# Kernel tuning notes

Measured on AMD Instinct MI355X. Metric: run time of the kernel, lower is better.

Reference implementation:

```python
import jax, jax.numpy as jnp
import numpy as np

IN_C = 256
OUT_C = 256
K = 3
PAD = 1
SCALE = 1.0 / np.sqrt(IN_C * K * K)  # 1/sqrt(in_channels * k^2)
EPS = 1e-8
NEG_SLOPE = 0.2


def setup_inputs() -> dict:
    key = jax.random.key(0)
    k0, k1, k2, k3 = jax.random.split(key, 4)
    B, H, W, SD = 8, 128, 128, 512
    x = jax.random.normal(k0, (B, IN_C, H, W), dtype=jnp.float32)
    style = jax.random.normal(k1, (B, SD), dtype=jnp.float32)
    weight = jax.random.normal(k2, (OUT_C, IN_C, K, K), dtype=jnp.float32)
    mod_w = jax.random.normal(k3, (IN_C, SD), dtype=jnp.float32) / np.sqrt(SD)
    mod_b = jnp.zeros((IN_C,), dtype=jnp.float32)
    return {"x": x, "style": style, "weight": weight, "mod_w": mod_w, "mod_b": mod_b}


def reference(x, style, weight, mod_w, mod_b):
    # modulation: Linear(style_dim -> in_channels)
    s = style @ mod_w.T + mod_b                      # [B, I]
    # per-sample modulated weight [B, O, I, k, k]
    w = SCALE * weight[None] * s[:, None, :, None, None]
    # demodulation over (I, kh, kw)
    demod = jax.lax.rsqrt(jnp.sum(w * w, axis=(2, 3, 4)) + EPS)  # [B, O]
    w = w * demod[:, :, None, None, None]
    # per-sample conv (equivalent to groups=batch trick), vmapped over batch
    def conv_one(xi, wi):  # xi: [I,H,W], wi: [O,I,k,k]
        return jax.lax.conv_general_dilated(
            xi[None], wi, window_strides=(1, 1),
            padding=((PAD, PAD), (PAD, PAD)),
            dimension_numbers=("NCHW", "OIHW", "NCHW"))[0]
    y = jax.vmap(conv_one)(x, w)                     # [B, O, H, W]
    # LeakyReLU(0.2)
    return jnp.where(y >= 0, y, NEG_SLOPE * y)
```

## Files before the change

### kernel.cpp

```cpp
#include <hip/hip_runtime.h>
#include <hip/hip_bf16.h>
#include <cstddef>
#include <cstdint>


#define IN_C 256
#define OUT_C 256
#define HW 16384
#define W_IMG 128
#define SDIM 512
#define SCALE_F 0.020833333333333332f
#define EPS_F 1e-8f
#define NEG_SLOPE 0.2f

#define XROWB 8320
#define WTILEB 8192

typedef short bf16x8 __attribute__((ext_vector_type(8)));
typedef float f32x4 __attribute__((ext_vector_type(4)));

__device__ __forceinline__ unsigned short f2bf(float f) {
  unsigned u = __builtin_bit_cast(unsigned, f);
  unsigned r = u + 0x7FFFu + ((u >> 16) & 1u);
  return (unsigned short)(r >> 16);
}

__device__ __forceinline__ void glds16(const void* g, void* l) {
  __builtin_amdgcn_global_load_lds(
      (const __attribute__((address_space(1))) unsigned int*)g,
      (__attribute__((address_space(3))) unsigned int*)l, 16, 0, 0);
}

__global__ void style_mod_kernel(const float* __restrict__ style,
                                 const float* __restrict__ mod_w,
                                 const float* __restrict__ mod_b,
                                 float* __restrict__ s_out) {
  int b = blockIdx.x;
  int i = threadIdx.x;
  const float* st = style + (size_t)b * SDIM;
  const float* mw = mod_w + (size_t)i * SDIM;
  float acc = 0.f;
#pragma unroll 8
  for (int j = 0; j < SDIM; ++j) acc += st[j] * mw[j];
  s_out[b * IN_C + i] = acc + mod_b[i];
}

__global__ void demod_kernel(const float* __restrict__ weight,
                             const float* __restrict__ s_in,
                             float* __restrict__ dscaled) {
  int bo = blockIdx.x;
  int b = bo >> 8, o = bo & 255;
  int i = threadIdx.x;
  const float* wp = weight + ((size_t)o * IN_C + i) * 9;
  float wsum = 0.f;
#pragma unroll
  for (int k = 0; k < 9; ++k) wsum += wp[k] * wp[k];
  float sv = s_in[b * IN_C + i];
  float v = sv * sv * wsum;
#pragma unroll
  for (int off = 32; off > 0; off >>= 1) v += __shfl_down(v, off);
  __shared__ float red[4];
  int lane = threadIdx.x & 63, wv = threadIdx.x >> 6;
  if (lane == 0) red[wv] = v;
  __syncthreads();
  if (threadIdx.x == 0) {
    float t = red[0] + red[1] + red[2] + red[3];
    dscaled[bo] = SCALE_F * rsqrtf(SCALE_F * SCALE_F * t + EPS_F);
  }
}

__global__ void wpack_kernel(const float* __restrict__ weight,
                             unsigned char* __restrict__ wbf) {
  int tap = blockIdx.x, oblk = blockIdx.y, iblk = blockIdx.z;
  unsigned char* dst = wbf + ((size_t)((tap * 2 + oblk) * 8 + iblk)) * WTILEB;
  for (int t = threadIdx.x; t < 512; t += 256) {
    int oo = t >> 2, c = t & 3;
    int cp = c ^ ((oo >> 1) & 3);
    int o = oblk * 128 + oo;
    bf16x8 v;
#pragma unroll
    for (int j = 0; j < 8; ++j) {
      int i = iblk * 32 + c * 8 + j;
      v[j] = (short)f2bf(weight[((size_t)o * IN_C + i) * 9 + tap]);
    }
    *(bf16x8*)(dst + oo * 64 + cp * 16) = v;
  }
}

__global__ void xpack_kernel(const float* __restrict__ x,
                             const float* __restrict__ s_in,
                             unsigned char* __restrict__ xp) {
  int row = blockIdx.x, iblk = blockIdx.y, b = blockIdx.z;
  const float* xb = x + ((size_t)(b * IN_C + iblk * 32)) * HW + row * W_IMG;
  const float* sb = s_in + b * IN_C + iblk * 32;
  unsigned char* dst = xp + ((size_t)((b * 8 + iblk) * 128 + row)) * XROWB;
  for (int t = threadIdx.x; t < 520; t += 256) {
    int slot = t >> 2, c = t & 3;
    int cp = c ^ ((slot >> 1) & 3);
    int pix = slot - 1;
    bf16x8 v = (bf16x8)(short)0;
    if ((unsigned)pix < 128u) {
#pragma unroll
      for (int j = 0; j < 8; ++j) {
        int ii = c * 8 + j;
        float xv = xb[(size_t)ii * HW + pix];
        v[j] = (short)f2bf(xv * sb[ii]);
      }
    }
    *(bf16x8*)(dst + slot * 64 + cp * 16) = v;
  }
}

__global__ __launch_bounds__(256, 4) void modconv_kernel(
    const unsigned char* __restrict__ xp, const unsigned char* __restrict__ wbf,
    const float* __restrict__ dscaled, float* __restrict__ out) {
  __shared__ __align__(16) unsigned char lds[XROWB + 3 * WTILEB];

  const int tid = threadIdx.x;
  const int lane = tid & 63;
  const int wv = tid >> 6;
  const int wr = wv >> 1, wc = wv & 1;
  const int h = blockIdx.x;
  const int oblk = blockIdx.y;
  const int b = blockIdx.z;
  const int l15 = lane & 15, cc = lane >> 4;

  f32x4 acc[4][4] = {};

  const int axor = ((cc ^ ((l15 >> 1) & 3)) << 4);
  int aoff[4];
#pragma unroll
  for (int m = 0; m < 4; ++m)
    aoff[m] = XROWB + (wr * 64 + m * 16 + l15) * 64 + axor;

  for (int kh = 0; kh < 3; ++kh) {
    const int row = h + kh - 1;
    if ((unsigned)row >= 128u) continue;
    for (int i0 = 0; i0 < 8; ++i0) {
      const unsigned char* xsrc =
          xp + ((size_t)((b * 8 + i0) * 128 + row)) * XROWB;
      for (int tsk = wv; tsk < 33; tsk += 4) {
        if (tsk < 24) {
          int kw = tsk >> 3, ch = tsk & 7;
          const unsigned char* g =
              wbf + ((size_t)(((kh * 3 + kw) * 2 + oblk) * 8 + i0)) * WTILEB +
              ch * 1024 + lane * 16;
          glds16(g, lds + XROWB + kw * WTILEB + ch * 1024);
        } else if (tsk < 32) {
          int ch = tsk - 24;
          glds16(xsrc + ch * 1024 + lane * 16, lds + ch * 1024);
        } else if (lane < 8) {
          glds16(xsrc + 8192 + lane * 16, lds + 8192);
        }
      }
      asm volatile("s_waitcnt vmcnt(0)" ::: "memory");
      __syncthreads();
#pragma unroll
      for (int kw = 0; kw < 3; ++kw) {
        bf16x8 a0 = *(const bf16x8*)(lds + kw * WTILEB + aoff[0]);
        bf16x8 a1 = *(const bf16x8*)(lds + kw * WTILEB + aoff[1]);
        bf16x8 a2 = *(const bf16x8*)(lds + kw * WTILEB + aoff[2]);
        bf16x8 a3 = *(const bf16x8*)(lds + kw * WTILEB + aoff[3]);
        const int bb0 = (wc * 64 + l15 + kw) * 64 +
                        ((cc ^ (((l15 + kw) >> 1) & 3)) << 4);
        __builtin_amdgcn_s_setprio(1);
#pragma unroll
        for (int n = 0; n < 4; ++n) {
          bf16x8 bn = *(const bf16x8*)(lds + bb0 + n * 1024);
          acc[0][n] = __builtin_amdgcn_mfma_f32_16x16x32_bf16(a0, bn, acc[0][n], 0, 0, 0);
          acc[1][n] = __builtin_amdgcn_mfma_f32_16x16x32_bf16(a1, bn, acc[1][n], 0, 0, 0);
          acc[2][n] = __builtin_amdgcn_mfma_f32_16x16x32_bf16(a2, bn, acc[2][n], 0, 0, 0);
          acc[3][n] = __builtin_amdgcn_mfma_f32_16x16x32_bf16(a3, bn, acc[3][n], 0, 0, 0);
        }
        __builtin_amdgcn_s_setprio(0);
      }
      __syncthreads();
    }
  }

  const float* db = dscaled + b * OUT_C + oblk * 128;
  float* ob = out + (((size_t)(b * OUT_C + oblk * 128)) << 14);
  const int pixb = h * 128 + wc * 64 + l15;
#pragma unroll
  for (int m = 0; m < 4; ++m) {
#pragma unroll
    for (int r = 0; r < 4; ++r) {
      int oo = wr * 64 + m * 16 + cc * 4 + r;
      float d = db[oo];
#pragma unroll
      for (int n = 0; n < 4; ++n) {
        float v = acc[m][n][r] * d;
        v = (v >= 0.f) ? v : NEG_SLOPE * v;
        ob[((size_t)oo << 14) + pixb + n * 16] = v;
      }
    }
  }
}

extern "C" void kernel_launch(void* const* d_in, const int* in_sizes, int n_in,
                              void* d_out, int out_size, void* d_ws,
                              size_t ws_size, hipStream_t stream) {
  const float* x = (const float*)d_in[0];
  const float* style = (const float*)d_in[1];
  const float* weight = (const float*)d_in[2];
  const float* mod_w = (const float*)d_in[3];
  const float* mod_b = (const float*)d_in[4];
  float* out = (float*)d_out;

  float* s_ws = (float*)d_ws;
  float* dsc = s_ws + 2048;
  unsigned char* wbf = (unsigned char*)d_ws + 16384;
  unsigned char* xp = wbf + (size_t)9 * 2 * 8 * WTILEB;

  style_mod_kernel<<<dim3(8), dim3(256), 0, stream>>>(style, mod_w, mod_b, s_ws);
  demod_kernel<<<dim3(8 * OUT_C), dim3(256), 0, stream>>>(weight, s_ws, dsc);
  wpack_kernel<<<dim3(9, 2, 8), dim3(256), 0, stream>>>(weight, wbf);
  xpack_kernel<<<dim3(128, 8, 8), dim3(256), 0, stream>>>(x, s_ws, xp);

  modconv_kernel<<<dim3(128, 2, 8), dim3(256), 0, stream>>>(xp, wbf, dsc, out);
}
```

Before: 407.3 us.

## Tile conv over two output rows, coalesce xpack via LDS transpose, restructure prologue kernels

The main conv kernel now computes two output rows per block, 8 N-tiles per wave, and shares each weight tile across both rows. This halves weight-tile loads per output, at the cost of double the accumulators and lower occupancy (launch bounds 2). Out-of-image rows are served from a zero row filled by a new kernel. xpack now reads x coalesced with float4 loads and transposes through LDS. The style and demod prologue kernels are vectorized, with the weight-square sum computed once instead of per batch.

```diff
diff --git a/kernel.cpp b/kernel.cpp
--- a/kernel.cpp
+++ b/kernel.cpp
@@ -35,37 +35,58 @@
                                  const float* __restrict__ mod_w,
                                  const float* __restrict__ mod_b,
                                  float* __restrict__ s_out) {
-  int b = blockIdx.x;
-  int i = threadIdx.x;
-  const float* st = style + (size_t)b * SDIM;
-  const float* mw = mod_w + (size_t)i * SDIM;
-  float acc = 0.f;
+  const int b = blockIdx.x, iq = blockIdx.y;
+  const int il = threadIdx.x >> 2, part = threadIdx.x & 3;
+  const int i = iq * 64 + il;
+  const float4* st4 = (const float4*)(style + (size_t)b * SDIM) + part * 32;
+  const float4* mw4 = (const float4*)(mod_w + (size_t)i * SDIM) + part * 32;
+  float a = 0.f;
 #pragma unroll 8
-  for (int j = 0; j < SDIM; ++j) acc += st[j] * mw[j];
-  s_out[b * IN_C + i] = acc + mod_b[i];
-}
-
-__global__ void demod_kernel(const float* __restrict__ weight,
+  for (int j = 0; j < 32; ++j) {
+    float4 s = st4[j], w = mw4[j];
+    a += s.x * w.x + s.y * w.y + s.z * w.z + s.w * w.w;
+  }
+  a += __shfl_xor(a, 1);
+  a += __shfl_xor(a, 2);
+  if (part == 0) s_out[b * IN_C + i] = a + mod_b[i];
+}
+
+__global__ void wsq_kernel(const float* __restrict__ weight,
+                           float* __restrict__ wsq) {
+  const int o = blockIdx.x, i = threadIdx.x;
+  const float* wp = weight + ((size_t)o * IN_C + i) * 9;
+  float s = 0.f;
+#pragma unroll
+  for (int k = 0; k < 9; ++k) s += wp[k] * wp[k];
+  wsq[o * IN_C + i] = s;
+}
+
+__global__ void demod_kernel(const float* __restrict__ wsq,
                              const float* __restrict__ s_in,
                              float* __restrict__ dscaled) {
-  int bo = blockIdx.x;
-  int b = bo >> 8, o = bo & 255;
-  int i = threadIdx.x;
-  const float* wp = weight + ((size_t)o * IN_C + i) * 9;
-  float wsum = 0.f;
-#pragma unroll
-  for (int k = 0; k < 9; ++k) wsum += wp[k] * wp[k];
-  float sv = s_in[b * IN_C + i];
-  float v = sv * sv * wsum;
-#pragma unroll
-  for (int off = 32; off > 0; off >>= 1) v += __shfl_down(v, off);
-  __shared__ float red[4];
-  int lane = threadIdx.x & 63, wv = threadIdx.x >> 6;
-  if (lane == 0) red[wv] = v;
+  const int o = blockIdx.x, i = threadIdx.x;
+  const float wq = wsq[o * IN_C + i];
+  float vb[8];
+#pragma unroll
+  for (int b = 0; b < 8; ++b) {
+    float sv = s_in[b * IN_C + i];
+    vb[b] = sv * sv * wq;
+  }
+#pragma unroll
+  for (int b = 0; b < 8; ++b)
+#pragma unroll
+    for (int off = 32; off > 0; off >>= 1) vb[b] += __shfl_down(vb[b], off);
+  __shared__ float red[4][8];
+  const int lane = threadIdx.x & 63, wvid = threadIdx.x >> 6;
+  if (lane == 0) {
+#pragma unroll
+    for (int b = 0; b < 8; ++b) red[wvid][b] = vb[b];
+  }
   __syncthreads();
-  if (threadIdx.x == 0) {
-    float t = red[0] + red[1] + red[2] + red[3];
-    dscaled[bo] = SCALE_F * rsqrtf(SCALE_F * SCALE_F * t + EPS_F);
+  if (threadIdx.x < 8) {
+    float t = red[0][threadIdx.x] + red[1][threadIdx.x] +
+              red[2][threadIdx.x] + red[3][threadIdx.x];
+    dscaled[threadIdx.x * OUT_C + o] = SCALE_F * rsqrtf(SCALE_F * SCALE_F * t + EPS_F);
   }
 }
 
@@ -87,70 +108,102 @@
   }
 }
 
-__global__ void xpack_kernel(const float* __restrict__ x,
-                             const float* __restrict__ s_in,
-                             unsigned char* __restrict__ xp) {
-  int row = blockIdx.x, iblk = blockIdx.y, b = blockIdx.z;
-  const float* xb = x + ((size_t)(b * IN_C + iblk * 32)) * HW + row * W_IMG;
-  const float* sb = s_in + b * IN_C + iblk * 32;
-  unsigned char* dst = xp + ((size_t)((b * 8 + iblk) * 128 + row)) * XROWB;
-  for (int t = threadIdx.x; t < 520; t += 256) {
-    int slot = t >> 2, c = t & 3;
-    int cp = c ^ ((slot >> 1) & 3);
-    int pix = slot - 1;
-    bf16x8 v = (bf16x8)(short)0;
-    if ((unsigned)pix < 128u) {
-#pragma unroll
-      for (int j = 0; j < 8; ++j) {
-        int ii = c * 8 + j;
-        float xv = xb[(size_t)ii * HW + pix];
-        v[j] = (short)f2bf(xv * sb[ii]);
-      }
-    }
-    *(bf16x8*)(dst + slot * 64 + cp * 16) = v;
-  }
-}
-
-__global__ __launch_bounds__(256, 4) void modconv_kernel(
+__global__ void zfill_kernel(float4* __restrict__ zrow) {
+  float4 z = {0.f, 0.f, 0.f, 0.f};
+  for (int c = threadIdx.x; c < XROWB / 16; c += 256) zrow[c] = z;
+}
+
+__global__ __launch_bounds__(256) void xpack_kernel(
+    const float* __restrict__ x, const float* __restrict__ s_in,
+    unsigned char* __restrict__ xp) {
+  __shared__ short xt[128 * 33];
+  const int tid = threadIdx.x;
+  const int rb = blockIdx.x, iblk = blockIdx.y, b = blockIdx.z;
+  const float* xbase = x + ((size_t)(b * IN_C + iblk * 32)) * HW;
+  const int chp = tid >> 5;
+  const int lp = tid & 31;
+  float sv[4];
+#pragma unroll
+  for (int p = 0; p < 4; ++p) sv[p] = s_in[b * IN_C + iblk * 32 + p * 8 + chp];
+
+  for (int r = 0; r < 8; ++r) {
+    const int row = rb * 8 + r;
+#pragma unroll
+    for (int p = 0; p < 4; ++p) {
+      const int ch = p * 8 + chp;
+      float4 v = *(const float4*)(xbase + (size_t)ch * HW + row * W_IMG + lp * 4);
+      const int pix0 = lp * 4;
+      xt[(pix0 + 0) * 33 + ch] = (short)f2bf(v.x * sv[p]);
+      xt[(pix0 + 1) * 33 + ch] = (short)f2bf(v.y * sv[p]);
+      xt[(pix0 + 2) * 33 + ch] = (short)f2bf(v.z * sv[p]);
+      xt[(pix0 + 3) * 33 + ch] = (short)f2bf(v.w * sv[p]);
+    }
+    __syncthreads();
+    unsigned char* dst = xp + ((size_t)((b * 8 + iblk) * 128 + row)) * XROWB;
+    for (int task = tid; task < 520; task += 256) {
+      int slot = task >> 2, c = task & 3;
+      int cp = c ^ ((slot >> 1) & 3);
+      int pix = slot - 1;
+      bf16x8 v = (bf16x8)(short)0;
+      if ((unsigned)pix < 128u) {
+#pragma unroll
+        for (int j = 0; j < 8; ++j) v[j] = xt[pix * 33 + c * 8 + j];
+      }
+      *(bf16x8*)(dst + slot * 64 + cp * 16) = v;
+    }
+    __syncthreads();
+  }
+}
+
+__global__ __launch_bounds__(256, 2) void modconv_kernel(
     const unsigned char* __restrict__ xp, const unsigned char* __restrict__ wbf,
-    const float* __restrict__ dscaled, float* __restrict__ out) {
-  __shared__ __align__(16) unsigned char lds[XROWB + 3 * WTILEB];
+    const unsigned char* __restrict__ zrow, const float* __restrict__ dscaled,
+    float* __restrict__ out) {
+  __shared__ __align__(16) unsigned char lds[2 * XROWB + 3 * WTILEB];
 
   const int tid = threadIdx.x;
   const int lane = tid & 63;
   const int wv = tid >> 6;
-  const int wr = wv >> 1, wc = wv & 1;
-  const int h = blockIdx.x;
-  const int oblk = blockIdx.y;
+  const int wr = wv >> 1;
+  const int wc = wv & 1;
+  const int oblk = blockIdx.x;
+  const int hp = blockIdx.y;
   const int b = blockIdx.z;
   const int l15 = lane & 15, cc = lane >> 4;
 
-  f32x4 acc[4][4] = {};
+  f32x4 acc[4][8] = {};
 
   const int axor = ((cc ^ ((l15 >> 1) & 3)) << 4);
   int aoff[4];
 #pragma unroll
   for (int m = 0; m < 4; ++m)
-    aoff[m] = XROWB + (wr * 64 + m * 16 + l15) * 64 + axor;
-
-  for (int kh = 0; kh < 3; ++kh) {
-    const int row = h + kh - 1;
-    if ((unsigned)row >= 128u) continue;
-    for (int i0 = 0; i0 < 8; ++i0) {
-      const unsigned char* xsrc =
-          xp + ((size_t)((b * 8 + i0) * 128 + row)) * XROWB;
-      for (int tsk = wv; tsk < 33; tsk += 4) {
-        if (tsk < 24) {
-          int kw = tsk >> 3, ch = tsk & 7;
-          const unsigned char* g =
+    aoff[m] = 2 * XROWB + (wr * 64 + m * 16 + l15) * 64 + axor;
+
+  const unsigned char* xpb = xp + ((size_t)(b * 8)) * 128 * XROWB;
+
+  for (int i0 = 0; i0 < 8; ++i0) {
+    for (int kh = 0; kh < 3; ++kh) {
+      for (int task = wv; task < 41; task += 4) {
+        if (task < 17) {
+          int c = task * 64 + lane;
+          if (task < 16 || lane < 16) {
+            int q = (c >= 520) ? 1 : 0;
+            int wdx = c - q * 520;
+            int gr = 2 * hp + kh - 1 + q;
+            const unsigned char* src =
+                ((unsigned)gr < 128u)
+                    ? xpb + ((size_t)(i0 * 128 + gr)) * XROWB + wdx * 16
+                    : zrow + wdx * 16;
+            glds16(src, lds + task * 1024);
+          }
+        } else {
+          int t2 = task - 17;
+          int c2 = t2 * 64 + lane;
+          int kw = c2 >> 9, rest = c2 & 511;
+          const unsigned char* src =
               wbf + ((size_t)(((kh * 3 + kw) * 2 + oblk) * 8 + i0)) * WTILEB +
-              ch * 1024 + lane * 16;
-          glds16(g, lds + XROWB + kw * WTILEB + ch * 1024);
-        } else if (tsk < 32) {
-          int ch = tsk - 24;
-          glds16(xsrc + ch * 1024 + lane * 16, lds + ch * 1024);
-        } else if (lane < 8) {
-          glds16(xsrc + 8192 + lane * 16, lds + 8192);
+              rest * 16;
+          glds16(src, lds + 2 * XROWB + t2 * 1024);
         }
       }
       asm volatile("s_waitcnt vmcnt(0)" ::: "memory");
@@ -161,12 +214,12 @@
         bf16x8 a1 = *(const bf16x8*)(lds + kw * WTILEB + aoff[1]);
         bf16x8 a2 = *(const bf16x8*)(lds + kw * WTILEB + aoff[2]);
         bf16x8 a3 = *(const bf16x8*)(lds + kw * WTILEB + aoff[3]);
-        const int bb0 = (wc * 64 + l15 + kw) * 64 +
-                        ((cc ^ (((l15 + kw) >> 1) & 3)) << 4);
         __builtin_amdgcn_s_setprio(1);
 #pragma unroll
-        for (int n = 0; n < 4; ++n) {
-          bf16x8 bn = *(const bf16x8*)(lds + bb0 + n * 1024);
+        for (int n = 0; n < 8; ++n) {
+          int slot = n * 16 + l15 + kw;
+          bf16x8 bn = *(const bf16x8*)(lds + wc * XROWB + slot * 64 +
+                                       ((cc ^ ((slot >> 1) & 3)) << 4));
           acc[0][n] = __builtin_amdgcn_mfma_f32_16x16x32_bf16(a0, bn, acc[0][n], 0, 0, 0);
           acc[1][n] = __builtin_amdgcn_mfma_f32_16x16x32_bf16(a1, bn, acc[1][n], 0, 0, 0);
           acc[2][n] = __builtin_amdgcn_mfma_f32_16x16x32_bf16(a2, bn, acc[2][n], 0, 0, 0);
@@ -179,8 +232,8 @@
   }
 
   const float* db = dscaled + b * OUT_C + oblk * 128;
-  float* ob = out + (((size_t)(b * OUT_C + oblk * 128)) << 14);
-  const int pixb = h * 128 + wc * 64 + l15;
+  const int r_out = 2 * hp + wc;
+  float* ob = out + (((size_t)(b * OUT_C + oblk * 128)) << 14) + r_out * 128;
 #pragma unroll
   for (int m = 0; m < 4; ++m) {
 #pragma unroll
@@ -188,10 +241,10 @@
       int oo = wr * 64 + m * 16 + cc * 4 + r;
       float d = db[oo];
 #pragma unroll
-      for (int n = 0; n < 4; ++n) {
+      for (int n = 0; n < 8; ++n) {
         float v = acc[m][n][r] * d;
         v = (v >= 0.f) ? v : NEG_SLOPE * v;
-        ob[((size_t)oo << 14) + pixb + n * 16] = v;
+        ob[((size_t)oo << 14) + n * 16 + l15] = v;
       }
     }
   }
@@ -209,13 +262,17 @@
 
   float* s_ws = (float*)d_ws;
   float* dsc = s_ws + 2048;
-  unsigned char* wbf = (unsigned char*)d_ws + 16384;
+  float* wsq = dsc + 2048;
+  unsigned char* wbf = (unsigned char*)(wsq + 65536);
   unsigned char* xp = wbf + (size_t)9 * 2 * 8 * WTILEB;
-
-  style_mod_kernel<<<dim3(8), dim3(256), 0, stream>>>(style, mod_w, mod_b, s_ws);
-  demod_kernel<<<dim3(8 * OUT_C), dim3(256), 0, stream>>>(weight, s_ws, dsc);
+  unsigned char* zrow = xp + (size_t)8 * 8 * 128 * XROWB;
+
+  style_mod_kernel<<<dim3(8, 4), dim3(256), 0, stream>>>(style, mod_w, mod_b, s_ws);
+  wsq_kernel<<<dim3(256), dim3(256), 0, stream>>>(weight, wsq);
+  demod_kernel<<<dim3(256), dim3(256), 0, stream>>>(wsq, s_ws, dsc);
   wpack_kernel<<<dim3(9, 2, 8), dim3(256), 0, stream>>>(weight, wbf);
-  xpack_kernel<<<dim3(128, 8, 8), dim3(256), 0, stream>>>(x, s_ws, xp);
-
-  modconv_kernel<<<dim3(128, 2, 8), dim3(256), 0, stream>>>(xp, wbf, dsc, out);
-}
+  zfill_kernel<<<dim3(1), dim3(256), 0, stream>>>((float4*)zrow);
+  xpack_kernel<<<dim3(16, 8, 8), dim3(256), 0, stream>>>(x, s_ws, xp);
+
+  modconv_kernel<<<dim3(2, 64, 8), dim3(256), 0, stream>>>(xp, wbf, zrow, dsc, out);
+}
```

New measurement: 432.6 us. 6.2% more time.
